# Kernel tuning notes

Measured on AMD Instinct MI355X. Metric: run time of the kernel, lower is better.

The kernel has to match this reference:

```python
import jax, jax.numpy as jnp
import numpy as np

N_NODES = 100000
EPS = 1e-5


def _layernorm(h, gamma, beta):
    mu = jnp.mean(h, axis=-1, keepdims=True)
    var = jnp.mean(jnp.square(h - mu), axis=-1, keepdims=True)
    return (h - mu) * jax.lax.rsqrt(var + EPS) * gamma + beta


def _gcn_conv(x, W, b, row, col, inv_sqrt_deg):
    # PyG GCNConv: y = D^{-1/2} (A + I) D^{-1/2} (x W) + b, self-loops already in row/col
    xw = x @ W                                  # [N, C]
    norm = inv_sqrt_deg[row] * inv_sqrt_deg[col]  # [E+N]
    msg = xw[row] * norm[:, None]               # [E+N, C] gather
    agg = jax.ops.segment_sum(msg, col, num_segments=N_NODES)  # scatter-add
    return agg + b


def setup_inputs() -> dict:
    key = jax.random.key(0)
    ks = jax.random.split(key, 8)
    C = 256
    x = jax.random.normal(ks[0], (N_NODES, C), dtype=jnp.float32)
    all_edges = jax.random.randint(ks[1], (2, 1600000), 0, N_NODES, dtype=jnp.int32)
    s = 1.0 / np.sqrt(C)
    W1 = jax.random.uniform(ks[2], (C, C), jnp.float32, -s, s)
    b1 = jnp.zeros((C,), jnp.float32)
    W2 = jax.random.uniform(ks[3], (C, C), jnp.float32, -s, s)
    b2 = jnp.zeros((C,), jnp.float32)
    gamma = jnp.ones((C,), jnp.float32)
    beta = jnp.zeros((C,), jnp.float32)
    return {"x": x, "all_edges": all_edges, "W1": W1, "b1": b1,
            "W2": W2, "b2": b2, "gamma": gamma, "beta": beta}


def reference(x, all_edges, W1, b1, W2, b2, gamma, beta):
    # add self-loops
    loops = jnp.arange(N_NODES, dtype=all_edges.dtype)
    row = jnp.concatenate([all_edges[0], loops])
    col = jnp.concatenate([all_edges[1], loops])
    deg = jax.ops.segment_sum(jnp.ones_like(col, dtype=x.dtype), col,
                              num_segments=N_NODES)
    inv_sqrt_deg = jnp.where(deg > 0, jax.lax.rsqrt(deg), 0.0)

    z1 = jax.nn.relu(_layernorm(_gcn_conv(x, W1, b1, row, col, inv_sqrt_deg), gamma, beta))
    z2 = jax.nn.relu(_layernorm(_gcn_conv(z1, W2, b2, row, col, inv_sqrt_deg), gamma, beta))
    return (z1, z2)
```

## Files before the change

kernel.cpp:

```cpp
#include <hip/hip_runtime.h>
#include <cstdint>

#define C_DIM 256
#define EPS 1e-5f

typedef __attribute__((ext_vector_type(8))) short short8;
typedef __attribute__((ext_vector_type(4))) float f32x4;

__device__ __forceinline__ ushort f2bf(float f) {
  uint32_t u = __float_as_uint(f);
  u = (u + 0x7fffu + ((u >> 16) & 1u)) >> 16;
  return (ushort)u;
}
__device__ __forceinline__ float bflo(uint32_t p) { return __uint_as_float(p << 16); }
__device__ __forceinline__ float bfhi(uint32_t p) { return __uint_as_float(p & 0xffff0000u); }

__global__ void k_count(const int* __restrict__ col, int E, int* cnt) {
  int e = blockIdx.x * blockDim.x + threadIdx.x;
  if (e < E) atomicAdd(&cnt[col[e]], 1);
}

__global__ void k_isd(int* cnt, float* isd, int n) {
  int i = blockIdx.x * blockDim.x + threadIdx.x;
  if (i < n) { isd[i] = rsqrtf((float)(cnt[i] + 1)); cnt[i] = 0; }
}

__global__ void k_scan1(const int* __restrict__ cnt, int* excl, int* bsum, int n) {
  __shared__ int s[1024];
  int i = blockIdx.x * 1024 + threadIdx.x;
  int v = (i < n) ? cnt[i] : 0;
  s[threadIdx.x] = v;
  __syncthreads();
  for (int off = 1; off < 1024; off <<= 1) {
    int t = (threadIdx.x >= off) ? s[threadIdx.x - off] : 0;
    __syncthreads();
    s[threadIdx.x] += t;
    __syncthreads();
  }
  if (i < n) excl[i] = s[threadIdx.x] - v;
  if (threadIdx.x == 1023) bsum[blockIdx.x] = s[1023];
}

__global__ void k_scan2(int* bsum, int nb) {
  __shared__ int s[1024];
  int v = (threadIdx.x < nb) ? bsum[threadIdx.x] : 0;
  s[threadIdx.x] = v;
  __syncthreads();
  for (int off = 1; off < 1024; off <<= 1) {
    int t = (threadIdx.x >= off) ? s[threadIdx.x - off] : 0;
    __syncthreads();
    s[threadIdx.x] += t;
    __syncthreads();
  }
  if (threadIdx.x < nb) bsum[threadIdx.x] = s[threadIdx.x] - v;
}

__global__ void k_scan3(int* excl, const int* __restrict__ bsum, int n, int E) {
  int i = blockIdx.x * 1024 + threadIdx.x;
  if (i < n) excl[i] += bsum[blockIdx.x];
  if (i == 0) excl[n] = E;
}

__global__ void k_fill(const int* __restrict__ row, const int* __restrict__ col, int E,
                       const int* __restrict__ row_ptr, int* cursor,
                       const float* __restrict__ isd, int2* __restrict__ edat) {
  int e = blockIdx.x * blockDim.x + threadIdx.x;
  if (e < E) {
    int d = col[e], s = row[e];
    int p = row_ptr[d] + atomicAdd(&cursor[d], 1);
    edat[p] = make_int2(s, __float_as_int(isd[s] * isd[d]));
  }
}

__global__ void k_cvt_x(const float* __restrict__ x, ushort* __restrict__ xb, int n4) {
  int i = blockIdx.x * blockDim.x + threadIdx.x;
  if (i < n4) {
    float4 v = ((const float4*)x)[i];
    ushort4 o;
    o.x = f2bf(v.x); o.y = f2bf(v.y); o.z = f2bf(v.z); o.w = f2bf(v.w);
    ((ushort4*)xb)[i] = o;
  }
}

__global__ void k_cvt_w(const float* __restrict__ W1, const float* __restrict__ W2,
                        ushort* __restrict__ Wt1, ushort* __restrict__ Wt2) {
  int i = blockIdx.x * blockDim.x + threadIdx.x;
  int n = i >> 8, k = i & 255;
  Wt1[i] = f2bf(W1[k * 256 + n]);
  Wt2[i] = f2bf(W2[k * 256 + n]);
}

__global__ __launch_bounds__(256) void k_gemm_bf16(const ushort* __restrict__ A,
                                                   const ushort* __restrict__ Wt,
                                                   ushort* __restrict__ Cb, int M) {
  __shared__ ushort As[128 * 64];
  __shared__ ushort Bs[128 * 64];
  const int tid = threadIdx.x;
  const int wave = tid >> 6, lane = tid & 63;
  const int bm = blockIdx.x * 128;
  const int bn = blockIdx.y * 128;
  const int wm = (wave >> 1) * 64, wn = (wave & 1) * 64;

  f32x4 acc[4][4] = {};

  const int r_off = lane >> 3;
  const int cc = lane & 7;

  for (int k0 = 0; k0 < C_DIM; k0 += 64) {
#pragma unroll
    for (int j = 0; j < 4; j++) {
      int rl = wave * 32 + j * 8 + r_off;
      int c = cc ^ (rl & 7);
      int gm = bm + rl; if (gm >= M) gm = M - 1;
      const ushort* ga = &A[(size_t)gm * C_DIM + k0 + c * 8];
      ushort* la = &As[(size_t)(wave * 32 + j * 8) * 64];
      __builtin_amdgcn_global_load_lds((const __attribute__((address_space(1))) void*)ga,
                                       (__attribute__((address_space(3))) void*)la, 16, 0, 0);
      const ushort* gb = &Wt[(size_t)(bn + rl) * C_DIM + k0 + c * 8];
      ushort* lb = &Bs[(size_t)(wave * 32 + j * 8) * 64];
      __builtin_amdgcn_global_load_lds((const __attribute__((address_space(1))) void*)gb,
                                       (__attribute__((address_space(3))) void*)lb, 16, 0, 0);
    }
    __syncthreads();
#pragma unroll
    for (int s = 0; s < 2; s++) {
      short8 af[4], bfr[4];
#pragma unroll
      for (int t = 0; t < 4; t++) {
        int ra = wm + t * 16 + (lane & 15);
        int ca = s * 4 + (lane >> 4);
        af[t] = *(const short8*)&As[ra * 64 + ((ca ^ (ra & 7)) << 3)];
        int rb = wn + t * 16 + (lane & 15);
        bfr[t] = *(const short8*)&Bs[rb * 64 + ((ca ^ (rb & 7)) << 3)];
      }
#pragma unroll
      for (int mt = 0; mt < 4; mt++)
#pragma unroll
        for (int nt = 0; nt < 4; nt++)
          acc[mt][nt] = __builtin_amdgcn_mfma_f32_16x16x32_bf16(af[mt], bfr[nt], acc[mt][nt], 0, 0, 0);
    }
    __syncthreads();
  }

#pragma unroll
  for (int mt = 0; mt < 4; mt++) {
#pragma unroll
    for (int nt = 0; nt < 4; nt++) {
      int col = bn + wn + nt * 16 + (lane & 15);
      int row0 = bm + wm + mt * 16 + ((lane >> 4) << 2);
#pragma unroll
      for (int r = 0; r < 4; r++) {
        int row = row0 + r;
        if (row < M) Cb[(size_t)row * C_DIM + col] = f2bf(acc[mt][nt][r]);
      }
    }
  }
}

__global__ __launch_bounds__(256) void k_agg_ln(const ushort* __restrict__ xwb,
    const int2* __restrict__ edat, const int* __restrict__ row_ptr,
    const float* __restrict__ isd,
    const float* __restrict__ bias, const float* __restrict__ gamma,
    const float* __restrict__ beta, float* __restrict__ out,
    ushort* __restrict__ outb, int n) {
  int i = blockIdx.x * 4 + (threadIdx.x >> 6);
  int lane = threadIdx.x & 63;
  if (i >= n) return;
  const uint2* xw2 = (const uint2*)xwb;

  float si = isd[i];
  float sn = si * si;
  uint2 p = xw2[(size_t)i * 64 + lane];
  float a0 = bflo(p.x) * sn, a1 = bfhi(p.x) * sn;
  float a2 = bflo(p.y) * sn, a3 = bfhi(p.y) * sn;

  int e0 = row_ptr[i], e1 = row_ptr[i + 1];
  int e = e0;
  for (; e + 3 < e1; e += 4) {
    int2 ed0 = edat[e], ed1 = edat[e + 1], ed2 = edat[e + 2], ed3 = edat[e + 3];
    uint2 v0 = xw2[(size_t)ed0.x * 64 + lane];
    uint2 v1 = xw2[(size_t)ed1.x * 64 + lane];
    uint2 v2 = xw2[(size_t)ed2.x * 64 + lane];
    uint2 v3 = xw2[(size_t)ed3.x * 64 + lane];
    float w0 = __int_as_float(ed0.y), w1 = __int_as_float(ed1.y);
    float w2 = __int_as_float(ed2.y), w3 = __int_as_float(ed3.y);
    a0 += bflo(v0.x) * w0 + bflo(v1.x) * w1 + bflo(v2.x) * w2 + bflo(v3.x) * w3;
    a1 += bfhi(v0.x) * w0 + bfhi(v1.x) * w1 + bfhi(v2.x) * w2 + bfhi(v3.x) * w3;
    a2 += bflo(v0.y) * w0 + bflo(v1.y) * w1 + bflo(v2.y) * w2 + bflo(v3.y) * w3;
    a3 += bfhi(v0.y) * w0 + bfhi(v1.y) * w1 + bfhi(v2.y) * w2 + bfhi(v3.y) * w3;
  }
  for (; e < e1; e++) {
    int2 ed = edat[e];
    float w0 = __int_as_float(ed.y);
    uint2 v0 = xw2[(size_t)ed.x * 64 + lane];
    a0 += bflo(v0.x) * w0; a1 += bfhi(v0.x) * w0;
    a2 += bflo(v0.y) * w0; a3 += bfhi(v0.y) * w0;
  }

  float4 bv = ((const float4*)bias)[lane];
  a0 += bv.x; a1 += bv.y; a2 += bv.z; a3 += bv.w;

  float sum = a0 + a1 + a2 + a3;
  float sq = a0 * a0 + a1 * a1 + a2 * a2 + a3 * a3;
#pragma unroll
  for (int off = 32; off >= 1; off >>= 1) {
    sum += __shfl_xor(sum, off, 64);
    sq += __shfl_xor(sq, off, 64);
  }
  float mu = sum * (1.0f / C_DIM);
  float var = sq * (1.0f / C_DIM) - mu * mu;
  float rs = rsqrtf(var + EPS);

  float4 g = ((const float4*)gamma)[lane];
  float4 bt = ((const float4*)beta)[lane];
  float4 o;
  o.x = fmaxf((a0 - mu) * rs * g.x + bt.x, 0.0f);
  o.y = fmaxf((a1 - mu) * rs * g.y + bt.y, 0.0f);
  o.z = fmaxf((a2 - mu) * rs * g.z + bt.z, 0.0f);
  o.w = fmaxf((a3 - mu) * rs * g.w + bt.w, 0.0f);
  ((float4*)out)[(size_t)i * 64 + lane] = o;

  if (outb) {
    uint2 q;
    q.x = (uint32_t)f2bf(o.x) | ((uint32_t)f2bf(o.y) << 16);
    q.y = (uint32_t)f2bf(o.z) | ((uint32_t)f2bf(o.w) << 16);
    ((uint2*)outb)[(size_t)i * 64 + lane] = q;
  }
}

extern "C" void kernel_launch(void* const* d_in, const int* in_sizes, int n_in,
                              void* d_out, int out_size, void* d_ws, size_t ws_size,
                              hipStream_t stream) {
  const float* x = (const float*)d_in[0];
  const int* edges = (const int*)d_in[1];
  const float* W1 = (const float*)d_in[2];
  const float* b1 = (const float*)d_in[3];
  const float* W2 = (const float*)d_in[4];
  const float* b2 = (const float*)d_in[5];
  const float* gamma = (const float*)d_in[6];
  const float* beta = (const float*)d_in[7];

  int N = in_sizes[0] / C_DIM;
  int E = in_sizes[1] / 2;
  const int* row = edges;
  const int* col = edges + E;

  char* ws = (char*)d_ws;
  size_t off = 0;
  auto alloc = [&](size_t bytes) -> void* {
    void* p = ws + off;
    off = (off + bytes + 255) & ~(size_t)255;
    return p;
  };
  ushort* xwb = (ushort*)alloc((size_t)N * C_DIM * 2);
  ushort* xb  = (ushort*)alloc((size_t)N * C_DIM * 2);
  ushort* Wt1 = (ushort*)alloc(65536 * 2);
  ushort* Wt2 = (ushort*)alloc(65536 * 2);
  int* cnt = (int*)alloc((size_t)N * 4);
  float* isd = (float*)alloc((size_t)N * 4);
  int* row_ptr = (int*)alloc((size_t)(N + 1) * 4);
  int nb = (N + 1023) / 1024;
  int* bsum = (int*)alloc((size_t)nb * 4);
  int2* edat = (int2*)alloc((size_t)E * 8);

  float* z1 = (float*)d_out;
  float* z2 = (float*)d_out + (size_t)N * C_DIM;

  int n4 = N * C_DIM / 4;
  k_cvt_x<<<(n4 + 255) / 256, 256, 0, stream>>>(x, xb, n4);
  k_cvt_w<<<256, 256, 0, stream>>>(W1, W2, Wt1, Wt2);

  hipMemsetAsync(cnt, 0, (size_t)N * 4, stream);
  k_count<<<(E + 255) / 256, 256, 0, stream>>>(col, E, cnt);
  k_scan1<<<nb, 1024, 0, stream>>>(cnt, row_ptr, bsum, N);
  k_scan2<<<1, 1024, 0, stream>>>(bsum, nb);
  k_scan3<<<nb, 1024, 0, stream>>>(row_ptr, bsum, N, E);
  k_isd<<<(N + 255) / 256, 256, 0, stream>>>(cnt, isd, N);
  k_fill<<<(E + 255) / 256, 256, 0, stream>>>(row, col, E, row_ptr, cnt, isd, edat);

  dim3 ggrid((N + 127) / 128, 2);
  int agg_blocks = (N + 3) / 4;

  k_gemm_bf16<<<ggrid, 256, 0, stream>>>(xb, Wt1, xwb, N);
  k_agg_ln<<<agg_blocks, 256, 0, stream>>>(xwb, edat, row_ptr, isd, b1, gamma, beta, z1, xb, N);
  k_gemm_bf16<<<ggrid, 256, 0, stream>>>(xb, Wt2, xwb, N);
  k_agg_ln<<<agg_blocks, 256, 0, stream>>>(xwb, edat, row_ptr, isd, b2, gamma, beta, z2, nullptr, N);
}
```

Baseline: 740.2 us.

## Reorder GCN layer to aggregate first, then fuse GEMM with bias/LayerNorm/ReLU

Uses the identity Â(XW) = (ÂX)W to run the sparse aggregation on the bf16 inputs first and the dense GEMM afterwards. The GEMM now covers the full 256-wide output row per block (512 threads), so bias, LayerNorm and ReLU can be fused into its epilogue through a shared-memory row reduction. This drops the separate full-row LN pass and the extra xw round trip. The cost is an extra bf16 rounding of the aggregated features before the GEMM, plus a larger block with more registers, which may lower occupancy.

```diff
diff --git a/kernel.cpp b/kernel.cpp
--- a/kernel.cpp
+++ b/kernel.cpp
@@ -90,87 +90,17 @@
   Wt2[i] = f2bf(W2[k * 256 + n]);
 }
 
-__global__ __launch_bounds__(256) void k_gemm_bf16(const ushort* __restrict__ A,
-                                                   const ushort* __restrict__ Wt,
-                                                   ushort* __restrict__ Cb, int M) {
-  __shared__ ushort As[128 * 64];
-  __shared__ ushort Bs[128 * 64];
-  const int tid = threadIdx.x;
-  const int wave = tid >> 6, lane = tid & 63;
-  const int bm = blockIdx.x * 128;
-  const int bn = blockIdx.y * 128;
-  const int wm = (wave >> 1) * 64, wn = (wave & 1) * 64;
-
-  f32x4 acc[4][4] = {};
-
-  const int r_off = lane >> 3;
-  const int cc = lane & 7;
-
-  for (int k0 = 0; k0 < C_DIM; k0 += 64) {
-#pragma unroll
-    for (int j = 0; j < 4; j++) {
-      int rl = wave * 32 + j * 8 + r_off;
-      int c = cc ^ (rl & 7);
-      int gm = bm + rl; if (gm >= M) gm = M - 1;
-      const ushort* ga = &A[(size_t)gm * C_DIM + k0 + c * 8];
-      ushort* la = &As[(size_t)(wave * 32 + j * 8) * 64];
-      __builtin_amdgcn_global_load_lds((const __attribute__((address_space(1))) void*)ga,
-                                       (__attribute__((address_space(3))) void*)la, 16, 0, 0);
-      const ushort* gb = &Wt[(size_t)(bn + rl) * C_DIM + k0 + c * 8];
-      ushort* lb = &Bs[(size_t)(wave * 32 + j * 8) * 64];
-      __builtin_amdgcn_global_load_lds((const __attribute__((address_space(1))) void*)gb,
-                                       (__attribute__((address_space(3))) void*)lb, 16, 0, 0);
-    }
-    __syncthreads();
-#pragma unroll
-    for (int s = 0; s < 2; s++) {
-      short8 af[4], bfr[4];
-#pragma unroll
-      for (int t = 0; t < 4; t++) {
-        int ra = wm + t * 16 + (lane & 15);
-        int ca = s * 4 + (lane >> 4);
-        af[t] = *(const short8*)&As[ra * 64 + ((ca ^ (ra & 7)) << 3)];
-        int rb = wn + t * 16 + (lane & 15);
-        bfr[t] = *(const short8*)&Bs[rb * 64 + ((ca ^ (rb & 7)) << 3)];
-      }
-#pragma unroll
-      for (int mt = 0; mt < 4; mt++)
-#pragma unroll
-        for (int nt = 0; nt < 4; nt++)
-          acc[mt][nt] = __builtin_amdgcn_mfma_f32_16x16x32_bf16(af[mt], bfr[nt], acc[mt][nt], 0, 0, 0);
-    }
-    __syncthreads();
-  }
-
-#pragma unroll
-  for (int mt = 0; mt < 4; mt++) {
-#pragma unroll
-    for (int nt = 0; nt < 4; nt++) {
-      int col = bn + wn + nt * 16 + (lane & 15);
-      int row0 = bm + wm + mt * 16 + ((lane >> 4) << 2);
-#pragma unroll
-      for (int r = 0; r < 4; r++) {
-        int row = row0 + r;
-        if (row < M) Cb[(size_t)row * C_DIM + col] = f2bf(acc[mt][nt][r]);
-      }
-    }
-  }
-}
-
-__global__ __launch_bounds__(256) void k_agg_ln(const ushort* __restrict__ xwb,
+__global__ __launch_bounds__(256) void k_agg(const ushort* __restrict__ xb,
     const int2* __restrict__ edat, const int* __restrict__ row_ptr,
-    const float* __restrict__ isd,
-    const float* __restrict__ bias, const float* __restrict__ gamma,
-    const float* __restrict__ beta, float* __restrict__ out,
-    ushort* __restrict__ outb, int n) {
+    const float* __restrict__ isd, ushort* __restrict__ axb, int n) {
   int i = blockIdx.x * 4 + (threadIdx.x >> 6);
   int lane = threadIdx.x & 63;
   if (i >= n) return;
-  const uint2* xw2 = (const uint2*)xwb;
+  const uint2* x2 = (const uint2*)xb;
 
   float si = isd[i];
   float sn = si * si;
-  uint2 p = xw2[(size_t)i * 64 + lane];
+  uint2 p = x2[(size_t)i * 64 + lane];
   float a0 = bflo(p.x) * sn, a1 = bfhi(p.x) * sn;
   float a2 = bflo(p.y) * sn, a3 = bfhi(p.y) * sn;
 
@@ -178,10 +108,10 @@
   int e = e0;
   for (; e + 3 < e1; e += 4) {
     int2 ed0 = edat[e], ed1 = edat[e + 1], ed2 = edat[e + 2], ed3 = edat[e + 3];
-    uint2 v0 = xw2[(size_t)ed0.x * 64 + lane];
-    uint2 v1 = xw2[(size_t)ed1.x * 64 + lane];
-    uint2 v2 = xw2[(size_t)ed2.x * 64 + lane];
-    uint2 v3 = xw2[(size_t)ed3.x * 64 + lane];
+    uint2 v0 = x2[(size_t)ed0.x * 64 + lane];
+    uint2 v1 = x2[(size_t)ed1.x * 64 + lane];
+    uint2 v2 = x2[(size_t)ed2.x * 64 + lane];
+    uint2 v3 = x2[(size_t)ed3.x * 64 + lane];
     float w0 = __int_as_float(ed0.y), w1 = __int_as_float(ed1.y);
     float w2 = __int_as_float(ed2.y), w3 = __int_as_float(ed3.y);
     a0 += bflo(v0.x) * w0 + bflo(v1.x) * w1 + bflo(v2.x) * w2 + bflo(v3.x) * w3;
@@ -192,39 +122,148 @@
   for (; e < e1; e++) {
     int2 ed = edat[e];
     float w0 = __int_as_float(ed.y);
-    uint2 v0 = xw2[(size_t)ed.x * 64 + lane];
+    uint2 v0 = x2[(size_t)ed.x * 64 + lane];
     a0 += bflo(v0.x) * w0; a1 += bfhi(v0.x) * w0;
     a2 += bflo(v0.y) * w0; a3 += bfhi(v0.y) * w0;
   }
 
-  float4 bv = ((const float4*)bias)[lane];
-  a0 += bv.x; a1 += bv.y; a2 += bv.z; a3 += bv.w;
-
-  float sum = a0 + a1 + a2 + a3;
-  float sq = a0 * a0 + a1 * a1 + a2 * a2 + a3 * a3;
-#pragma unroll
-  for (int off = 32; off >= 1; off >>= 1) {
-    sum += __shfl_xor(sum, off, 64);
-    sq += __shfl_xor(sq, off, 64);
-  }
-  float mu = sum * (1.0f / C_DIM);
-  float var = sq * (1.0f / C_DIM) - mu * mu;
-  float rs = rsqrtf(var + EPS);
-
-  float4 g = ((const float4*)gamma)[lane];
-  float4 bt = ((const float4*)beta)[lane];
-  float4 o;
-  o.x = fmaxf((a0 - mu) * rs * g.x + bt.x, 0.0f);
-  o.y = fmaxf((a1 - mu) * rs * g.y + bt.y, 0.0f);
-  o.z = fmaxf((a2 - mu) * rs * g.z + bt.z, 0.0f);
-  o.w = fmaxf((a3 - mu) * rs * g.w + bt.w, 0.0f);
-  ((float4*)out)[(size_t)i * 64 + lane] = o;
-
-  if (outb) {
-    uint2 q;
-    q.x = (uint32_t)f2bf(o.x) | ((uint32_t)f2bf(o.y) << 16);
-    q.y = (uint32_t)f2bf(o.z) | ((uint32_t)f2bf(o.w) << 16);
-    ((uint2*)outb)[(size_t)i * 64 + lane] = q;
+  uint2 q;
+  q.x = (uint32_t)f2bf(a0) | ((uint32_t)f2bf(a1) << 16);
+  q.y = (uint32_t)f2bf(a2) | ((uint32_t)f2bf(a3) << 16);
+  ((uint2*)axb)[(size_t)i * 64 + lane] = q;
+}
+
+__global__ __launch_bounds__(512) void k_gemm_ln(const ushort* __restrict__ A,
+    const ushort* __restrict__ Wt, const float* __restrict__ bias,
+    const float* __restrict__ gamma, const float* __restrict__ beta,
+    float* __restrict__ out, ushort* __restrict__ outb, int M) {
+  __shared__ ushort As[128 * 64];
+  __shared__ ushort Bs[256 * 64];
+  const int tid = threadIdx.x;
+  const int wave = tid >> 6, lane = tid & 63;
+  const int bm = blockIdx.x * 128;
+  const int wm = (wave >> 2) * 64, wn = (wave & 3) * 64;
+
+  f32x4 acc[4][4] = {};
+  const int r_off = lane >> 3;
+  const int cc = lane & 7;
+
+  for (int k0 = 0; k0 < C_DIM; k0 += 64) {
+#pragma unroll
+    for (int j = 0; j < 6; j++) {
+      int q = wave * 6 + j;
+      if (q < 16) {
+        int rl = q * 8 + r_off;
+        int c = cc ^ (rl & 7);
+        int gm = bm + rl; if (gm >= M) gm = M - 1;
+        const ushort* ga = &A[(size_t)gm * C_DIM + k0 + c * 8];
+        ushort* la = &As[q * 8 * 64];
+        __builtin_amdgcn_global_load_lds((const __attribute__((address_space(1))) void*)ga,
+                                         (__attribute__((address_space(3))) void*)la, 16, 0, 0);
+      } else {
+        int rl = (q - 16) * 8 + r_off;
+        int c = cc ^ (rl & 7);
+        const ushort* gb = &Wt[(size_t)rl * C_DIM + k0 + c * 8];
+        ushort* lb = &Bs[(q - 16) * 8 * 64];
+        __builtin_amdgcn_global_load_lds((const __attribute__((address_space(1))) void*)gb,
+                                         (__attribute__((address_space(3))) void*)lb, 16, 0, 0);
+      }
+    }
+    __syncthreads();
+#pragma unroll
+    for (int s = 0; s < 2; s++) {
+      short8 af[4], bfr[4];
+      int ca = s * 4 + (lane >> 4);
+#pragma unroll
+      for (int t = 0; t < 4; t++) {
+        int ra = wm + t * 16 + (lane & 15);
+        af[t] = *(const short8*)&As[ra * 64 + ((ca ^ (ra & 7)) << 3)];
+        int rb = wn + t * 16 + (lane & 15);
+        bfr[t] = *(const short8*)&Bs[rb * 64 + ((ca ^ (rb & 7)) << 3)];
+      }
+#pragma unroll
+      for (int mt = 0; mt < 4; mt++)
+#pragma unroll
+        for (int nt = 0; nt < 4; nt++)
+          acc[mt][nt] = __builtin_amdgcn_mfma_f32_16x16x32_bf16(af[mt], bfr[nt], acc[mt][nt], 0, 0, 0);
+    }
+    __syncthreads();
+  }
+
+#pragma unroll
+  for (int nt = 0; nt < 4; nt++) {
+    float bcol = bias[wn + nt * 16 + (lane & 15)];
+#pragma unroll
+    for (int mt = 0; mt < 4; mt++)
+#pragma unroll
+      for (int r = 0; r < 4; r++)
+        acc[mt][nt][r] += bcol;
+  }
+
+  float psum[4][4], psq[4][4];
+#pragma unroll
+  for (int mt = 0; mt < 4; mt++)
+#pragma unroll
+    for (int r = 0; r < 4; r++) {
+      float s = 0.0f, q2 = 0.0f;
+#pragma unroll
+      for (int nt = 0; nt < 4; nt++) {
+        float v = acc[mt][nt][r];
+        s += v; q2 += v * v;
+      }
+#pragma unroll
+      for (int off = 1; off <= 8; off <<= 1) {
+        s += __shfl_xor(s, off, 64);
+        q2 += __shfl_xor(q2, off, 64);
+      }
+      psum[mt][r] = s; psq[mt][r] = q2;
+    }
+
+  float* red = (float*)As;
+  if ((lane & 15) == 0) {
+    int qr = lane >> 4;
+#pragma unroll
+    for (int mt = 0; mt < 4; mt++)
+#pragma unroll
+      for (int r = 0; r < 4; r++) {
+        int row = wm + mt * 16 + qr * 4 + r;
+        red[row * 4 + (wave & 3)] = psum[mt][r];
+        red[512 + row * 4 + (wave & 3)] = psq[mt][r];
+      }
+  }
+  __syncthreads();
+
+  float mu[4][4], rs[4][4];
+#pragma unroll
+  for (int mt = 0; mt < 4; mt++)
+#pragma unroll
+    for (int r = 0; r < 4; r++) {
+      int row = wm + mt * 16 + (lane >> 4) * 4 + r;
+      float s  = red[row * 4 + 0] + red[row * 4 + 1] + red[row * 4 + 2] + red[row * 4 + 3];
+      float q2 = red[512 + row * 4 + 0] + red[512 + row * 4 + 1] +
+                 red[512 + row * 4 + 2] + red[512 + row * 4 + 3];
+      float m = s * (1.0f / C_DIM);
+      mu[mt][r] = m;
+      rs[mt][r] = rsqrtf(q2 * (1.0f / C_DIM) - m * m + EPS);
+    }
+
+#pragma unroll
+  for (int nt = 0; nt < 4; nt++) {
+    int col = wn + nt * 16 + (lane & 15);
+    float g = gamma[col], bt = beta[col];
+#pragma unroll
+    for (int mt = 0; mt < 4; mt++) {
+      int row0 = bm + wm + mt * 16 + ((lane >> 4) << 2);
+#pragma unroll
+      for (int r = 0; r < 4; r++) {
+        int row = row0 + r;
+        if (row < M) {
+          float v = fmaxf((acc[mt][nt][r] - mu[mt][r]) * rs[mt][r] * g + bt, 0.0f);
+          __builtin_nontemporal_store(v, &out[(size_t)row * C_DIM + col]);
+          if (outb) outb[(size_t)row * C_DIM + col] = f2bf(v);
+        }
+      }
+    }
   }
 }
 
@@ -252,8 +291,8 @@
     off = (off + bytes + 255) & ~(size_t)255;
     return p;
   };
-  ushort* xwb = (ushort*)alloc((size_t)N * C_DIM * 2);
   ushort* xb  = (ushort*)alloc((size_t)N * C_DIM * 2);
+  ushort* axb = (ushort*)alloc((size_t)N * C_DIM * 2);
   ushort* Wt1 = (ushort*)alloc(65536 * 2);
   ushort* Wt2 = (ushort*)alloc(65536 * 2);
   int* cnt = (int*)alloc((size_t)N * 4);
@@ -278,11 +317,11 @@
   k_isd<<<(N + 255) / 256, 256, 0, stream>>>(cnt, isd, N);
   k_fill<<<(E + 255) / 256, 256, 0, stream>>>(row, col, E, row_ptr, cnt, isd, edat);
 
-  dim3 ggrid((N + 127) / 128, 2);
   int agg_blocks = (N + 3) / 4;
-
-  k_gemm_bf16<<<ggrid, 256, 0, stream>>>(xb, Wt1, xwb, N);
-  k_agg_ln<<<agg_blocks, 256, 0, stream>>>(xwb, edat, row_ptr, isd, b1, gamma, beta, z1, xb, N);
-  k_gemm_bf16<<<ggrid, 256, 0, stream>>>(xb, Wt2, xwb, N);
-  k_agg_ln<<<agg_blocks, 256, 0, stream>>>(xwb, edat, row_ptr, isd, b2, gamma, beta, z2, nullptr, N);
-}
+  dim3 ggrid((N + 127) / 128);
+
+  k_agg<<<agg_blocks, 256, 0, stream>>>(xb, edat, row_ptr, isd, axb, N);
+  k_gemm_ln<<<ggrid, 512, 0, stream>>>(axb, Wt1, b1, gamma, beta, z1, xb, N);
+  k_agg<<<agg_blocks, 256, 0, stream>>>(xb, edat, row_ptr, isd, axb, N);
+  k_gemm_ln<<<ggrid, 512, 0, stream>>>(axb, Wt2, b2, gamma, beta, z2, nullptr, N);
+}
```

New measurement: 805.3 us. +8.8%, slower.

## Store GEMM output in column slabs and aggregate per-XCD slab for cache locality

Applied to the files above, without the earlier changes.

The GEMM now writes its output in 16-column slabs (slab-major layout). Aggregation is split into a separate kernel in which each block group, keyed by blockIdx mod 8 (presumably mapped to an XCD), gathers from only two slabs, so each slab's working set (about 3.2 MB) can stay in that die's L2. The edge data shrinks to source indices only, and the weights are recomputed from isd. LayerNorm runs as its own kernel reading the slab-layout aggregate and uses nontemporal stores. The split adds an extra round trip of the N×256 bf16 intermediate and an extra launch per layer, and the speedup depends on the block-to-XCD mapping assumption holding.

```diff
diff --git a/kernel.cpp b/kernel.cpp
--- a/kernel.cpp
+++ b/kernel.cpp
@@ -63,12 +63,12 @@
 
 __global__ void k_fill(const int* __restrict__ row, const int* __restrict__ col, int E,
                        const int* __restrict__ row_ptr, int* cursor,
-                       const float* __restrict__ isd, int2* __restrict__ edat) {
+                       int* __restrict__ es) {
   int e = blockIdx.x * blockDim.x + threadIdx.x;
   if (e < E) {
     int d = col[e], s = row[e];
     int p = row_ptr[d] + atomicAdd(&cursor[d], 1);
-    edat[p] = make_int2(s, __float_as_int(isd[s] * isd[d]));
+    es[p] = s;
   }
 }
 
@@ -92,7 +92,7 @@
 
 __global__ __launch_bounds__(256) void k_gemm_bf16(const ushort* __restrict__ A,
                                                    const ushort* __restrict__ Wt,
-                                                   ushort* __restrict__ Cb, int M) {
+                                                   ushort* __restrict__ Cc, int M) {
   __shared__ ushort As[128 * 64];
   __shared__ ushort Bs[128 * 64];
   const int tid = threadIdx.x;
@@ -146,59 +146,84 @@
   for (int mt = 0; mt < 4; mt++) {
 #pragma unroll
     for (int nt = 0; nt < 4; nt++) {
-      int col = bn + wn + nt * 16 + (lane & 15);
+      int slab = (bn + wn) / 16 + nt;
       int row0 = bm + wm + mt * 16 + ((lane >> 4) << 2);
 #pragma unroll
       for (int r = 0; r < 4; r++) {
         int row = row0 + r;
-        if (row < M) Cb[(size_t)row * C_DIM + col] = f2bf(acc[mt][nt][r]);
+        if (row < M) Cc[((size_t)slab * M + row) * 16 + (lane & 15)] = f2bf(acc[mt][nt][r]);
       }
     }
   }
 }
 
-__global__ __launch_bounds__(256) void k_agg_ln(const ushort* __restrict__ xwb,
-    const int2* __restrict__ edat, const int* __restrict__ row_ptr,
-    const float* __restrict__ isd,
+__global__ __launch_bounds__(256) void k_agg_x(const ushort* __restrict__ xwc,
+    const int* __restrict__ es, const int* __restrict__ row_ptr,
+    const float* __restrict__ isd, ushort* __restrict__ axc, int n) {
+  const int xcd = blockIdx.x & 7;
+  const int sub = blockIdx.x >> 3;
+  const int NB = (n + 255) >> 8;
+  int base = sub * NB;
+  int end = base + NB; if (end > n) end = n;
+  const int grp = threadIdx.x >> 2;
+  const int cl = threadIdx.x & 3;
+
+#pragma unroll
+  for (int h = 0; h < 2; h++) {
+    const int g = xcd * 2 + h;
+    const ushort* slab = xwc + (size_t)g * n * 16;
+    ushort* oslab = axc + (size_t)g * n * 16;
+
+    for (int i = base + grp; i < end; i += 64) {
+      float si = isd[i];
+      float sn = si * si;
+      uint2 p = *(const uint2*)&slab[(size_t)i * 16 + cl * 4];
+      float a0 = bflo(p.x) * sn, a1 = bfhi(p.x) * sn;
+      float a2 = bflo(p.y) * sn, a3 = bfhi(p.y) * sn;
+
+      int e1 = row_ptr[i + 1];
+      int e = row_ptr[i];
+      for (; e + 3 < e1; e += 4) {
+        int s0 = es[e], s1 = es[e + 1], s2 = es[e + 2], s3 = es[e + 3];
+        uint2 v0 = *(const uint2*)&slab[(size_t)s0 * 16 + cl * 4];
+        uint2 v1 = *(const uint2*)&slab[(size_t)s1 * 16 + cl * 4];
+        uint2 v2 = *(const uint2*)&slab[(size_t)s2 * 16 + cl * 4];
+        uint2 v3 = *(const uint2*)&slab[(size_t)s3 * 16 + cl * 4];
+        float w0 = isd[s0] * si, w1 = isd[s1] * si;
+        float w2 = isd[s2] * si, w3 = isd[s3] * si;
+        a0 += bflo(v0.x) * w0 + bflo(v1.x) * w1 + bflo(v2.x) * w2 + bflo(v3.x) * w3;
+        a1 += bfhi(v0.x) * w0 + bfhi(v1.x) * w1 + bfhi(v2.x) * w2 + bfhi(v3.x) * w3;
+        a2 += bflo(v0.y) * w0 + bflo(v1.y) * w1 + bflo(v2.y) * w2 + bflo(v3.y) * w3;
+        a3 += bfhi(v0.y) * w0 + bfhi(v1.y) * w1 + bfhi(v2.y) * w2 + bfhi(v3.y) * w3;
+      }
+      for (; e < e1; e++) {
+        int s0 = es[e];
+        float w0 = isd[s0] * si;
+        uint2 v0 = *(const uint2*)&slab[(size_t)s0 * 16 + cl * 4];
+        a0 += bflo(v0.x) * w0; a1 += bfhi(v0.x) * w0;
+        a2 += bflo(v0.y) * w0; a3 += bfhi(v0.y) * w0;
+      }
+
+      uint2 q;
+      q.x = (uint32_t)f2bf(a0) | ((uint32_t)f2bf(a1) << 16);
+      q.y = (uint32_t)f2bf(a2) | ((uint32_t)f2bf(a3) << 16);
+      *(uint2*)&oslab[(size_t)i * 16 + cl * 4] = q;
+    }
+  }
+}
+
+__global__ __launch_bounds__(256) void k_ln(const ushort* __restrict__ axc,
     const float* __restrict__ bias, const float* __restrict__ gamma,
     const float* __restrict__ beta, float* __restrict__ out,
     ushort* __restrict__ outb, int n) {
   int i = blockIdx.x * 4 + (threadIdx.x >> 6);
   int lane = threadIdx.x & 63;
   if (i >= n) return;
-  const uint2* xw2 = (const uint2*)xwb;
-
-  float si = isd[i];
-  float sn = si * si;
-  uint2 p = xw2[(size_t)i * 64 + lane];
-  float a0 = bflo(p.x) * sn, a1 = bfhi(p.x) * sn;
-  float a2 = bflo(p.y) * sn, a3 = bfhi(p.y) * sn;
-
-  int e0 = row_ptr[i], e1 = row_ptr[i + 1];
-  int e = e0;
-  for (; e + 3 < e1; e += 4) {
-    int2 ed0 = edat[e], ed1 = edat[e + 1], ed2 = edat[e + 2], ed3 = edat[e + 3];
-    uint2 v0 = xw2[(size_t)ed0.x * 64 + lane];
-    uint2 v1 = xw2[(size_t)ed1.x * 64 + lane];
-    uint2 v2 = xw2[(size_t)ed2.x * 64 + lane];
-    uint2 v3 = xw2[(size_t)ed3.x * 64 + lane];
-    float w0 = __int_as_float(ed0.y), w1 = __int_as_float(ed1.y);
-    float w2 = __int_as_float(ed2.y), w3 = __int_as_float(ed3.y);
-    a0 += bflo(v0.x) * w0 + bflo(v1.x) * w1 + bflo(v2.x) * w2 + bflo(v3.x) * w3;
-    a1 += bfhi(v0.x) * w0 + bfhi(v1.x) * w1 + bfhi(v2.x) * w2 + bfhi(v3.x) * w3;
-    a2 += bflo(v0.y) * w0 + bflo(v1.y) * w1 + bflo(v2.y) * w2 + bflo(v3.y) * w3;
-    a3 += bfhi(v0.y) * w0 + bfhi(v1.y) * w1 + bfhi(v2.y) * w2 + bfhi(v3.y) * w3;
-  }
-  for (; e < e1; e++) {
-    int2 ed = edat[e];
-    float w0 = __int_as_float(ed.y);
-    uint2 v0 = xw2[(size_t)ed.x * 64 + lane];
-    a0 += bflo(v0.x) * w0; a1 += bfhi(v0.x) * w0;
-    a2 += bflo(v0.y) * w0; a3 += bfhi(v0.y) * w0;
-  }
-
+
+  uint2 p = *(const uint2*)&axc[((size_t)(lane >> 2) * n + i) * 16 + (lane & 3) * 4];
   float4 bv = ((const float4*)bias)[lane];
-  a0 += bv.x; a1 += bv.y; a2 += bv.z; a3 += bv.w;
+  float a0 = bflo(p.x) + bv.x, a1 = bfhi(p.x) + bv.y;
+  float a2 = bflo(p.y) + bv.z, a3 = bfhi(p.y) + bv.w;
 
   float sum = a0 + a1 + a2 + a3;
   float sq = a0 * a0 + a1 * a1 + a2 * a2 + a3 * a3;
@@ -213,17 +238,17 @@
 
   float4 g = ((const float4*)gamma)[lane];
   float4 bt = ((const float4*)beta)[lane];
-  float4 o;
-  o.x = fmaxf((a0 - mu) * rs * g.x + bt.x, 0.0f);
-  o.y = fmaxf((a1 - mu) * rs * g.y + bt.y, 0.0f);
-  o.z = fmaxf((a2 - mu) * rs * g.z + bt.z, 0.0f);
-  o.w = fmaxf((a3 - mu) * rs * g.w + bt.w, 0.0f);
-  ((float4*)out)[(size_t)i * 64 + lane] = o;
+  f32x4 o;
+  o[0] = fmaxf((a0 - mu) * rs * g.x + bt.x, 0.0f);
+  o[1] = fmaxf((a1 - mu) * rs * g.y + bt.y, 0.0f);
+  o[2] = fmaxf((a2 - mu) * rs * g.z + bt.z, 0.0f);
+  o[3] = fmaxf((a3 - mu) * rs * g.w + bt.w, 0.0f);
+  __builtin_nontemporal_store(o, (f32x4*)&((float*)out)[((size_t)i * 64 + lane) * 4]);
 
   if (outb) {
     uint2 q;
-    q.x = (uint32_t)f2bf(o.x) | ((uint32_t)f2bf(o.y) << 16);
-    q.y = (uint32_t)f2bf(o.z) | ((uint32_t)f2bf(o.w) << 16);
+    q.x = (uint32_t)f2bf(o[0]) | ((uint32_t)f2bf(o[1]) << 16);
+    q.y = (uint32_t)f2bf(o[2]) | ((uint32_t)f2bf(o[3]) << 16);
     ((uint2*)outb)[(size_t)i * 64 + lane] = q;
   }
 }
@@ -252,8 +277,9 @@
     off = (off + bytes + 255) & ~(size_t)255;
     return p;
   };
-  ushort* xwb = (ushort*)alloc((size_t)N * C_DIM * 2);
   ushort* xb  = (ushort*)alloc((size_t)N * C_DIM * 2);
+  ushort* xwc = (ushort*)alloc((size_t)N * C_DIM * 2);
+  ushort* axc = (ushort*)alloc((size_t)N * C_DIM * 2);
   ushort* Wt1 = (ushort*)alloc(65536 * 2);
   ushort* Wt2 = (ushort*)alloc(65536 * 2);
   int* cnt = (int*)alloc((size_t)N * 4);
@@ -261,7 +287,7 @@
   int* row_ptr = (int*)alloc((size_t)(N + 1) * 4);
   int nb = (N + 1023) / 1024;
   int* bsum = (int*)alloc((size_t)nb * 4);
-  int2* edat = (int2*)alloc((size_t)E * 8);
+  int* es = (int*)alloc((size_t)E * 4);
 
   float* z1 = (float*)d_out;
   float* z2 = (float*)d_out + (size_t)N * C_DIM;
@@ -270,19 +296,21 @@
   k_cvt_x<<<(n4 + 255) / 256, 256, 0, stream>>>(x, xb, n4);
   k_cvt_w<<<256, 256, 0, stream>>>(W1, W2, Wt1, Wt2);
 
-  hipMemsetAsync(cnt, 0, (size_t)N * 4, stream);
+  (void)hipMemsetAsync(cnt, 0, (size_t)N * 4, stream);
   k_count<<<(E + 255) / 256, 256, 0, stream>>>(col, E, cnt);
   k_scan1<<<nb, 1024, 0, stream>>>(cnt, row_ptr, bsum, N);
   k_scan2<<<1, 1024, 0, stream>>>(bsum, nb);
   k_scan3<<<nb, 1024, 0, stream>>>(row_ptr, bsum, N, E);
   k_isd<<<(N + 255) / 256, 256, 0, stream>>>(cnt, isd, N);
-  k_fill<<<(E + 255) / 256, 256, 0, stream>>>(row, col, E, row_ptr, cnt, isd, edat);
+  k_fill<<<(E + 255) / 256, 256, 0, stream>>>(row, col, E, row_ptr, cnt, es);
 
   dim3 ggrid((N + 127) / 128, 2);
-  int agg_blocks = (N + 3) / 4;
-
-  k_gemm_bf16<<<ggrid, 256, 0, stream>>>(xb, Wt1, xwb, N);
-  k_agg_ln<<<agg_blocks, 256, 0, stream>>>(xwb, edat, row_ptr, isd, b1, gamma, beta, z1, xb, N);
-  k_gemm_bf16<<<ggrid, 256, 0, stream>>>(xb, Wt2, xwb, N);
-  k_agg_ln<<<agg_blocks, 256, 0, stream>>>(xwb, edat, row_ptr, isd, b2, gamma, beta, z2, nullptr, N);
-}
+  int ln_blocks = (N + 3) / 4;
+
+  k_gemm_bf16<<<ggrid, 256, 0, stream>>>(xb, Wt1, xwc, N);
+  k_agg_x<<<2048, 256, 0, stream>>>(xwc, es, row_ptr, isd, axc, N);
+  k_ln<<<ln_blocks, 256, 0, stream>>>(axc, b1, gamma, beta, z1, xb, N);
+  k_gemm_bf16<<<ggrid, 256, 0, stream>>>(xb, Wt2, xwc, N);
+  k_agg_x<<<2048, 256, 0, stream>>>(xwc, es, row_ptr, isd, axc, N);
+  k_ln<<<ln_blocks, 256, 0, stream>>>(axc, b2, gamma, beta, z2, nullptr, N);
+}
```

Measured after the change: 1.149 ms. 1.55x slower.
